# Kernel optimization log

Measured on AMD Instinct MI355X. Metric: run time of the kernel, lower is better.

Reference implementation:

```python
import jax, jax.numpy as jnp
import numpy as np
import math

B, S, H, DK, NB = 2, 128, 4, 128, 4
D = H * DK  # 512


def setup_inputs() -> dict:
    key = jax.random.key(0)
    ks = jax.random.split(key, 24)
    g = lambda i, sh, std=1.0: jax.random.normal(ks[i], sh, jnp.float32) * std
    u = lambda i, sh: jax.random.uniform(ks[i], sh, jnp.float32)
    return {
        "x_m": g(0, (B, S, D)), "x_c": g(1, (B, S, D)),
        "b_m": g(2, (B, S, D)), "b_c": g(3, (B, S, D)),
        "bb_m": g(4, (B, NB, NB, D)), "bb_c": u(5, (B, NB, NB, D)),
        "p_m": g(6, (B, S, D)), "p_c": u(7, (B, S, D)),
        "W_xm": g(8, (3, D, H, DK), 0.02), "W_xc": g(9, (3, D, H, DK), 0.02),
        "W_bm": g(10, (3, D, H, DK), 0.02), "W_bc": g(11, (3, D, H, DK), 0.02),
        "Wq1_w": g(12, (DK, DK), 0.05), "Wq1_b": g(13, (DK,), 0.02),
        "Wq2_w": g(14, (DK, DK), 0.05), "Wq2_b": g(15, (DK,), 0.02),
        "Wk1_w": g(16, (DK, DK), 0.05), "Wk1_b": g(17, (DK,), 0.02),
        "Wk2_w": g(18, (DK, DK), 0.05), "Wk2_b": g(19, (DK,), 0.02),
        "mean_w": g(20, (D, D), 0.02), "mean_b": jnp.zeros((D,), jnp.float32),
        "cov_w": g(21, (D, D), 0.02), "cov_b": jnp.zeros((D,), jnp.float32),
        "ln_w": jnp.ones((D,), jnp.float32), "ln_b": jnp.zeros((D,), jnp.float32),
        "b_seq": jax.random.randint(ks[22], (B, S), 0, NB),
    }


def _elu1(x):
    return jax.nn.elu(x) + 1.0


def _tri_sagp(m1, m2, m3, c1, c2, c3):
    # fuse three diagonal Gaussians by product-of-Gaussians (precision-weighted)
    eps = 1e-24
    p1 = 1.0 / jnp.clip(c1, eps)
    p2 = 1.0 / jnp.clip(c2, eps)
    p3 = 1.0 / jnp.clip(c3, eps)
    c = 1.0 / (p1 + p2 + p3)
    return c * (m1 * p1 + m2 * p2 + m3 * p3), c


def _ln(x, w, b):
    m = jnp.mean(x, -1, keepdims=True)
    v = jnp.mean((x - m) ** 2, -1, keepdims=True)
    return (x - m) / jnp.sqrt(v + 1e-12) * w + b


def _forward(x_m, x_c, b_m, b_c, bb_m, bb_c, p_m, p_c,
             W_xm, W_xc, W_bm, W_bc,
             Wq1_w, Wq1_b, Wq2_w, Wq2_b, Wk1_w, Wk1_b, Wk2_w, Wk2_b,
             mean_w, mean_b, cov_w, cov_b, ln_w, ln_b, b_seq):
    Bb, Ss, Dd = x_m.shape
    Hh, Dk = W_xm.shape[2], W_xm.shape[3]
    proj = lambda x, w: jnp.einsum('bnd,dhk->bhnk', x, w)
    q1 = proj(x_m, W_xm[0]) + proj(b_m, W_bm[0])
    k1 = proj(x_m, W_xm[1]) + proj(b_m, W_bm[1])
    v1 = proj(x_m, W_xm[2]) + proj(b_m, W_bm[2])
    q2 = _elu1(proj(x_c, W_xc[0]) + proj(b_c, W_bc[0]))
    k2 = _elu1(proj(x_c, W_xc[1]) + proj(b_c, W_bc[1]))
    v2 = _elu1(proj(x_c, W_xc[2]) + proj(b_c, W_bc[2]))
    nb = bb_m.shape[1]
    # [B,NB,NB,D] -> [B,H,NB,NB,DK]
    bbm = bb_m.reshape(Bb, nb, nb, Hh, Dk).transpose(0, 3, 1, 2, 4)
    bbc = bb_c.reshape(Bb, nb, nb, Hh, Dk).transpose(0, 3, 1, 2, 4)
    # out[b,h,i,j,:] = bbm[b,h,b_seq[b,j],b_seq[b,i],:]  (matches torch advanced indexing + permute)
    gather = jax.vmap(lambda bb, seq: bb[:, seq[None, :], seq[:, None], :])
    bbm_b = gather(bbm, b_seq)  # [B,H,S,S,DK]
    bbc_b = gather(bbc, b_seq)
    pm = p_m.reshape(Bb, Ss, Hh, Dk).transpose(0, 2, 1, 3)  # [B,H,S,DK]
    pc = p_c.reshape(Bb, Ss, Hh, Dk).transpose(0, 2, 1, 3)
    lin = lambda x, w, b: x @ w.T + b
    fQm, fQc = _tri_sagp(q1[:, :, :, None, :], lin(bbm_b, Wq1_w, Wq1_b),
                         lin(pm, Wq2_w, Wq2_b)[:, :, :, None, :],
                         q2[:, :, :, None, :], bbc_b, pc[:, :, :, None, :])
    fKm, fKc = _tri_sagp(k1[:, :, None, :, :], lin(bbm_b, Wk1_w, Wk1_b),
                         lin(pm, Wk2_w, Wk2_b)[:, :, None, :, :],
                         k2[:, :, None, :, :], bbc_b, pc[:, :, None, :, :])
    eps = 1e-24
    # 2-Wasserstein^2 between diagonal Gaussians (the 1x1 matmul form reduces to this)
    w2 = jnp.sum((fQm - fKm) ** 2, -1) + jnp.sum(
        (jnp.sqrt(jnp.clip(fQc, eps)) - jnp.sqrt(jnp.clip(fKc, eps))) ** 2, -1)
    scores = -w2 / math.sqrt(Dk)  # [B,H,S,S]
    probs = jax.nn.softmax(scores, axis=-1)
    mean_ctx = jnp.einsum('bhij,bhjk->bhik', probs, v1)
    cov_ctx = jnp.einsum('bhij,bhjk->bhik', probs ** 2, v2)
    mean_ctx = mean_ctx.transpose(0, 2, 1, 3).reshape(Bb, Ss, Dd)
    cov_ctx = cov_ctx.transpose(0, 2, 1, 3).reshape(Bb, Ss, Dd)
    mean_h = _ln(mean_ctx @ mean_w.T + mean_b + x_m, ln_w, ln_b)
    cov_h = _ln(cov_ctx @ cov_w.T + cov_b + x_c, ln_w, ln_b)
    return mean_h, cov_h, probs


def reference(x_m, x_c, b_m, b_c, bb_m, bb_c, p_m, p_c,
              W_xm, W_xc, W_bm, W_bc,
              Wq1_w, Wq1_b, Wq2_w, Wq2_b, Wk1_w, Wk1_b, Wk2_w, Wk2_b,
              mean_w, mean_b, cov_w, cov_b, ln_w, ln_b, b_seq):
    return _forward(x_m, x_c, b_m, b_c, bb_m, bb_c, p_m, p_c,
                    W_xm, W_xc, W_bm, W_bc,
                    Wq1_w, Wq1_b, Wq2_w, Wq2_b, Wk1_w, Wk1_b, Wk2_w, Wk2_b,
                    mean_w, mean_b, cov_w, cov_b, ln_w, ln_b, b_seq)
```

## Files before the change

kernel.cpp:

```cpp
#include <hip/hip_runtime.h>
#include <math.h>

#define B_ 2
#define S_ 128
#define H_ 4
#define DK_ 128
#define NB_ 4
#define D_ 512
#define M_ 256

typedef __attribute__((ext_vector_type(8))) short short8;
typedef __attribute__((ext_vector_type(4))) float float4v;

__device__ __forceinline__ float elu1(float x) {
    return (x > 0.f) ? (x + 1.f) : __expf(x);
}

__device__ __forceinline__ unsigned short f2bf(float f) {
    unsigned u = __float_as_uint(f);
    unsigned r = (u + 0x7FFFu + ((u >> 16) & 1u)) >> 16;
    return (unsigned short)r;
}


__global__ __launch_bounds__(256) void k_cvt_copy(
    const float* __restrict__ x_m, const float* __restrict__ b_m,
    const float* __restrict__ x_c, const float* __restrict__ b_c,
    const float* __restrict__ mean_w, const float* __restrict__ cov_w,
    unsigned short* __restrict__ A_m, unsigned short* __restrict__ A_c,
    unsigned short* __restrict__ wm_bf, unsigned short* __restrict__ wc_bf)
{
    const int t = threadIdx.x, job = blockIdx.y;
#pragma unroll
    for (int u = 0; u < 4; ++u) {
        int e = blockIdx.x * 1024 + u * 256 + t;
        float v;
        unsigned short* dst;
        if (job == 0) {
            int m = e >> 10, k = e & 1023;
            v = (k < 512) ? x_m[m * 512 + k] : b_m[m * 512 + k - 512];
            dst = A_m;
        } else if (job == 1) {
            int m = e >> 10, k = e & 1023;
            v = (k < 512) ? x_c[m * 512 + k] : b_c[m * 512 + k - 512];
            dst = A_c;
        } else if (job == 2) { v = mean_w[e]; dst = wm_bf; }
        else                 { v = cov_w[e];  dst = wc_bf; }
        dst[e] = f2bf(v);
    }
}

__global__ __launch_bounds__(256) void k_cvt_wt(
    const float* __restrict__ W_xm, const float* __restrict__ W_xc,
    const float* __restrict__ W_bm, const float* __restrict__ W_bc,
    unsigned short* __restrict__ Wt)
{
    const int o = blockIdx.z >> 1, part = blockIdx.z & 1;
    const float* src;
    if (part == 0) src = (o < 3) ? (W_xm + o * 262144) : (W_xc + (o - 3) * 262144);
    else           src = (o < 3) ? (W_bm + o * 262144) : (W_bc + (o - 3) * 262144);

    __shared__ unsigned short tile[32][33];
    const int tx = threadIdx.x & 31, ty = threadIdx.x >> 5;
    const int nt = blockIdx.x, kt = blockIdx.y;
#pragma unroll
    for (int u = 0; u < 4; ++u)
        tile[ty + u * 8][tx] = f2bf(src[(kt * 32 + ty + u * 8) * 512 + nt * 32 + tx]);
    __syncthreads();
    unsigned short* dst = Wt + o * 524288 + part * 512;
#pragma unroll
    for (int u = 0; u < 4; ++u)
        dst[(nt * 32 + ty + u * 8) * 1024 + kt * 32 + tx] = tile[tx][ty + u * 8];
}

__global__ __launch_bounds__(256) void k_mm(
    const unsigned short* __restrict__ A_m, const unsigned short* __restrict__ A_c,
    const unsigned short* __restrict__ Wt, float* __restrict__ qkv)
{
    const int t = threadIdx.x;
    const int wid = blockIdx.x * 4 + (t >> 6);
    const int lane = t & 63;
    const int o = wid >> 9;
    const int rem = wid & 511;
    const int nt = rem & 31, mt = rem >> 5;
    const int m0 = mt * 16, n0 = nt * 16;
    const int l15 = lane & 15, quad = lane >> 4;

    const unsigned short* A = (o < 3) ? A_m : A_c;
    const unsigned short* ap = A + (m0 + l15) * 1024 + quad * 8;
    const unsigned short* bp = Wt + o * 524288 + (n0 + l15) * 1024 + quad * 8;

    float4v acc0 = {0.f, 0.f, 0.f, 0.f};
    float4v acc1 = {0.f, 0.f, 0.f, 0.f};
#pragma unroll
    for (int k0 = 0; k0 < 1024; k0 += 64) {
        short8 a0 = *(const short8*)(ap + k0);
        short8 b0 = *(const short8*)(bp + k0);
        short8 a1 = *(const short8*)(ap + k0 + 32);
        short8 b1 = *(const short8*)(bp + k0 + 32);
        acc0 = __builtin_amdgcn_mfma_f32_16x16x32_bf16(a0, b0, acc0, 0, 0, 0);
        acc1 = __builtin_amdgcn_mfma_f32_16x16x32_bf16(a1, b1, acc1, 0, 0, 0);
    }

    float* dst = qkv + o * 131072;
#pragma unroll
    for (int r = 0; r < 4; ++r) {
        float v = acc0[r] + acc1[r];
        if (o >= 3) v = elu1(v);
        dst[(m0 + quad * 4 + r) * 512 + n0 + l15] = v;
    }
}

__global__ __launch_bounds__(128) void k_lin(
    const float* __restrict__ p_m, const float* __restrict__ bb_m,
    const float* __restrict__ Wq2, const float* __restrict__ bq2,
    const float* __restrict__ Wk2, const float* __restrict__ bk2,
    const float* __restrict__ Wq1, const float* __restrict__ bq1,
    const float* __restrict__ Wk1, const float* __restrict__ bk1,
    float* __restrict__ pq, float* __restrict__ pk,
    float* __restrict__ bbq, float* __restrict__ bbk)
{
    const int bx = blockIdx.x, t = threadIdx.x;
    const float *src, *Wm, *bias;
    float* dst;
    int row0;
    if (bx < 128)      { src = p_m;  Wm = Wq2; bias = bq2; dst = pq;  row0 = bx * 8; }
    else if (bx < 256) { src = p_m;  Wm = Wk2; bias = bk2; dst = pk;  row0 = (bx - 128) * 8; }
    else if (bx < 272) { src = bb_m; Wm = Wq1; bias = bq1; dst = bbq; row0 = (bx - 256) * 8; }
    else               { src = bb_m; Wm = Wk1; bias = bk1; dst = bbk; row0 = (bx - 272) * 8; }

    __shared__ float ps[8][128];
    __shared__ float wsh[128][33];

#pragma unroll
    for (int r = 0; r < 8; ++r) ps[r][t] = src[(row0 + r) * 128 + t];

    float acc[8];
#pragma unroll
    for (int r = 0; r < 8; ++r) acc[r] = 0.f;

    const int kc = t & 31, kr0 = t >> 5;
    for (int c0 = 0; c0 < 128; c0 += 32) {
        __syncthreads();
#pragma unroll 8
        for (int u = 0; u < 32; ++u)
            wsh[kr0 + u * 4][kc] = Wm[(kr0 + u * 4) * 128 + c0 + kc];
        __syncthreads();
#pragma unroll 8
        for (int k2 = 0; k2 < 32; ++k2) {
            float wv = wsh[t][k2];
#pragma unroll
            for (int r = 0; r < 8; ++r)
                acc[r] = fmaf(ps[r][c0 + k2], wv, acc[r]);
        }
    }

    float bv = bias[t];
#pragma unroll
    for (int r = 0; r < 8; ++r) dst[(row0 + r) * 128 + t] = acc[r] + bv;
}

__global__ __launch_bounds__(128) void k_fuse(
    const float* __restrict__ qkv, const float* __restrict__ pq,
    const float* __restrict__ pk, const float* __restrict__ bbq,
    const float* __restrict__ bbk, const float* __restrict__ bb_c,
    const float* __restrict__ p_c, const int* __restrict__ b_seq,
    float* __restrict__ fQm, float* __restrict__ fQs,
    float* __restrict__ fKm, float* __restrict__ fKs)
{
    const int t = threadIdx.x;
    const int ij = blockIdx.x;
    const int h = blockIdx.y;
    const int b = blockIdx.z >> 1;
    const int side = blockIdx.z & 1;
    const int d = h * 128 + t;
    const float eps = 1e-24f;
    const int base = (b * S_ + ij) * D_ + d;
    const int s_self = b_seq[b * S_ + ij];

    float m1, c1, m3;
    if (side == 0) { m1 = qkv[base];           c1 = qkv[3 * M_ * D_ + base]; m3 = pq[base]; }
    else           { m1 = qkv[M_ * D_ + base]; c1 = qkv[4 * M_ * D_ + base]; m3 = pk[base]; }
    float c3 = p_c[base];

    float p1 = 1.f / fmaxf(c1, eps);
    float p3 = 1.f / fmaxf(c3, eps);
    float mp13 = m1 * p1 + m3 * p3;
    const float* bbM = side ? bbk : bbq;

#pragma unroll
    for (int sv = 0; sv < 4; ++sv) {
        int n1 = side ? s_self : sv;
        int n2 = side ? sv : s_self;
        int idx = (b * 16 + n1 * 4 + n2) * 512 + d;
        float m2 = bbM[idx];
        float c2 = bb_c[idx];
        float p2 = 1.f / fmaxf(c2, eps);
        float cc = 1.f / (p1 + p2 + p3);
        float fm = cc * (mp13 + m2 * p2);
        float fs = sqrtf(fmaxf(cc, eps));
        if (side == 0) {
            int o = ((b * H_ + h) * S_ + ij) * 512 + sv * 128 + t;
            fQm[o] = fm; fQs[o] = fs;
        } else {
            int o = (((b * H_ + h) * 4 + sv) * S_ + ij) * 128 + t;
            fKm[o] = fm; fKs[o] = fs;
        }
    }
}

__global__ __launch_bounds__(128) void k_attn(
    const float* __restrict__ fQm, const float* __restrict__ fQs,
    const float* __restrict__ fKm, const float* __restrict__ fKs,
    const float* __restrict__ qkv, const int* __restrict__ b_seq,
    float* __restrict__ probs_out, unsigned short* __restrict__ mctxb,
    unsigned short* __restrict__ cctxb)
{
    const int t = threadIdx.x;
    const int i = blockIdx.x, h = blockIdx.y, b = blockIdx.z;

    __shared__ __attribute__((aligned(16))) float qm[4 * 132];
    __shared__ __attribute__((aligned(16))) float qs[4 * 132];
    __shared__ float red[4];
    __shared__ float pr[128], pr2[128];

    const int si = b_seq[b * S_ + i];
    const int sj = b_seq[b * S_ + t];
    const int qbase = ((b * H_ + h) * S_ + i) * 512;
#pragma unroll
    for (int u = 0; u < 4; ++u) {
        qm[u * 132 + t] = fQm[qbase + u * 128 + t];
        qs[u * 132 + t] = fQs[qbase + u * 128 + t];
    }
    __syncthreads();

    const int krow = (((b * H_ + h) * 4 + si) * S_ + t) * 128;
    const float4* kmp = (const float4*)(fKm + krow);
    const float4* ksp = (const float4*)(fKs + krow);

    float w2 = 0.f;
#pragma unroll 4
    for (int k4 = 0; k4 < 32; ++k4) {
        float4 km = kmp[k4];
        float4 ks = ksp[k4];
        float4 m = *(const float4*)&qm[sj * 132 + k4 * 4];
        float4 s = *(const float4*)&qs[sj * 132 + k4 * 4];
        float d0 = m.x - km.x, d1 = m.y - km.y, d2 = m.z - km.z, d3 = m.w - km.w;
        float e0 = s.x - ks.x, e1 = s.y - ks.y, e2 = s.z - ks.z, e3 = s.w - ks.w;
        w2 += d0 * d0 + d1 * d1 + d2 * d2 + d3 * d3
            + e0 * e0 + e1 * e1 + e2 * e2 + e3 * e3;
    }
    float score = -w2 * 0.08838834764831845f;

    float mx = score;
#pragma unroll
    for (int off = 32; off >= 1; off >>= 1) mx = fmaxf(mx, __shfl_xor(mx, off));
    if ((t & 63) == 0) red[t >> 6] = mx;
    __syncthreads();
    mx = fmaxf(red[0], red[1]);
    float e = __expf(score - mx);
    float sm = e;
#pragma unroll
    for (int off = 32; off >= 1; off >>= 1) sm += __shfl_xor(sm, off);
    if ((t & 63) == 0) red[2 + (t >> 6)] = sm;
    __syncthreads();
    float p = e / (red[2] + red[3]);

    probs_out[((b * H_ + h) * S_ + i) * S_ + t] = p;
    pr[t] = p;
    pr2[t] = p * p;
    __syncthreads();

    const float* v1 = qkv + 2 * M_ * D_ + (b * S_) * D_ + h * 128 + t;
    const float* v2 = qkv + 5 * M_ * D_ + (b * S_) * D_ + h * 128 + t;
    float am = 0.f, ac = 0.f;
#pragma unroll 8
    for (int j = 0; j < 128; ++j) {
        am = fmaf(pr[j], v1[j * D_], am);
        ac = fmaf(pr2[j], v2[j * D_], ac);
    }
    mctxb[(b * S_ + i) * D_ + h * 128 + t] = f2bf(am);
    cctxb[(b * S_ + i) * D_ + h * 128 + t] = f2bf(ac);
}

__global__ __launch_bounds__(256) void k_fin_mm(
    const unsigned short* __restrict__ mctxb, const unsigned short* __restrict__ cctxb,
    const unsigned short* __restrict__ wm_bf, const unsigned short* __restrict__ wc_bf,
    float* __restrict__ y_m, float* __restrict__ y_c)
{
    const int t = threadIdx.x;
    const int wid = blockIdx.x * 4 + (t >> 6);
    const int lane = t & 63;
    const int mat = wid >> 10;
    const int rem = wid & 1023;
    const int ks = rem >> 9;
    const int r2 = rem & 511;
    const int nt = r2 & 31, mt = r2 >> 5;
    const int m0 = mt * 16, n0 = nt * 16, kbase = ks * 256;
    const int l15 = lane & 15, quad = lane >> 4;

    const unsigned short* A = mat ? cctxb : mctxb;
    const unsigned short* Bw = mat ? wc_bf : wm_bf;
    float* y = mat ? y_c : y_m;

    const unsigned short* ap = A + (m0 + l15) * 512 + kbase + quad * 8;
    const unsigned short* bp = Bw + (n0 + l15) * 512 + kbase + quad * 8;

    float4v acc0 = {0.f, 0.f, 0.f, 0.f};
    float4v acc1 = {0.f, 0.f, 0.f, 0.f};
#pragma unroll
    for (int k0 = 0; k0 < 256; k0 += 64) {
        short8 a0 = *(const short8*)(ap + k0);
        short8 b0 = *(const short8*)(bp + k0);
        short8 a1 = *(const short8*)(ap + k0 + 32);
        short8 b1 = *(const short8*)(bp + k0 + 32);
        acc0 = __builtin_amdgcn_mfma_f32_16x16x32_bf16(a0, b0, acc0, 0, 0, 0);
        acc1 = __builtin_amdgcn_mfma_f32_16x16x32_bf16(a1, b1, acc1, 0, 0, 0);
    }
#pragma unroll
    for (int r = 0; r < 4; ++r)
        atomicAdd(&y[(m0 + quad * 4 + r) * 512 + n0 + l15], acc0[r] + acc1[r]);
}

__global__ __launch_bounds__(256) void k_ln(
    const float* __restrict__ y_m, const float* __restrict__ y_c,
    const float* __restrict__ mean_b, const float* __restrict__ cov_b,
    const float* __restrict__ x_m, const float* __restrict__ x_c,
    const float* __restrict__ ln_w, const float* __restrict__ ln_b,
    float* __restrict__ out)
{
    const int t = threadIdx.x;
    const int id = blockIdx.x;
    const int mat = id >> 8, row = id & 255;
    const float* yg = mat ? y_c : y_m;
    const float* bias = mat ? cov_b : mean_b;
    const float* res = mat ? x_c : x_m;
    const int base = row * 512;

    __shared__ float red[8];

    float y0 = yg[base + t] + bias[t] + res[base + t];
    float y1 = yg[base + 256 + t] + bias[256 + t] + res[base + 256 + t];
    float s = y0 + y1, ss = y0 * y0 + y1 * y1;
#pragma unroll
    for (int off = 32; off >= 1; off >>= 1) { s += __shfl_xor(s, off); ss += __shfl_xor(ss, off); }
    if ((t & 63) == 0) { red[t >> 6] = s; red[4 + (t >> 6)] = ss; }
    __syncthreads();
    float mu = (red[0] + red[1] + red[2] + red[3]) * (1.f / 512.f);
    float var = (red[4] + red[5] + red[6] + red[7]) * (1.f / 512.f) - mu * mu;
    float rstd = 1.f / sqrtf(var + 1e-12f);
    out[mat * 131072 + base + t] = (y0 - mu) * rstd * ln_w[t] + ln_b[t];
    out[mat * 131072 + base + 256 + t] = (y1 - mu) * rstd * ln_w[256 + t] + ln_b[256 + t];
}

extern "C" void kernel_launch(void* const* d_in, const int* in_sizes, int n_in,
                              void* d_out, int out_size, void* d_ws, size_t ws_size,
                              hipStream_t stream) {
    (void)in_sizes; (void)n_in; (void)out_size; (void)ws_size;
    const float* x_m   = (const float*)d_in[0];
    const float* x_c   = (const float*)d_in[1];
    const float* b_m   = (const float*)d_in[2];
    const float* b_c   = (const float*)d_in[3];
    const float* bb_m  = (const float*)d_in[4];
    const float* bb_c  = (const float*)d_in[5];
    const float* p_m   = (const float*)d_in[6];
    const float* p_c   = (const float*)d_in[7];
    const float* W_xm  = (const float*)d_in[8];
    const float* W_xc  = (const float*)d_in[9];
    const float* W_bm  = (const float*)d_in[10];
    const float* W_bc  = (const float*)d_in[11];
    const float* Wq1_w = (const float*)d_in[12];
    const float* Wq1_b = (const float*)d_in[13];
    const float* Wq2_w = (const float*)d_in[14];
    const float* Wq2_b = (const float*)d_in[15];
    const float* Wk1_w = (const float*)d_in[16];
    const float* Wk1_b = (const float*)d_in[17];
    const float* Wk2_w = (const float*)d_in[18];
    const float* Wk2_b = (const float*)d_in[19];
    const float* mean_w = (const float*)d_in[20];
    const float* mean_b = (const float*)d_in[21];
    const float* cov_w  = (const float*)d_in[22];
    const float* cov_b  = (const float*)d_in[23];
    const float* ln_w   = (const float*)d_in[24];
    const float* ln_b   = (const float*)d_in[25];
    const int*   b_seq  = (const int*)d_in[26];

    float* ws   = (float*)d_ws;
    float* qkv  = ws;
    float* pq   = ws + 786432;
    float* pk   = ws + 917504;
    float* bbq  = ws + 1048576;
    float* bbk  = ws + 1064960;
    float* fQm  = ws + 1081344;
    float* fQs  = ws + 1605632;
    float* fKm  = ws + 2129920;
    float* fKs  = ws + 2654208;
    float* y_m  = ws + 3178496;
    float* y_c  = ws + 3309568;
    unsigned short* A_m   = (unsigned short*)(ws + 3440640);
    unsigned short* A_c   = (unsigned short*)(ws + 3571712);
    unsigned short* Wt    = (unsigned short*)(ws + 3702784);
    unsigned short* wm_bf = (unsigned short*)(ws + 5275648);
    unsigned short* wc_bf = (unsigned short*)(ws + 5406720);
    unsigned short* mctxb = (unsigned short*)(ws + 5537792);
    unsigned short* cctxb = (unsigned short*)(ws + 5603328);
    float* out  = (float*)d_out;

    hipMemsetAsync(y_m, 0, 262144 * sizeof(float), stream);
    k_cvt_copy<<<dim3(256, 4), 256, 0, stream>>>(x_m, b_m, x_c, b_c, mean_w, cov_w,
                                                 A_m, A_c, wm_bf, wc_bf);
    k_cvt_wt<<<dim3(16, 16, 12), 256, 0, stream>>>(W_xm, W_xc, W_bm, W_bc, Wt);
    k_mm<<<dim3(768), 256, 0, stream>>>(A_m, A_c, Wt, qkv);
    k_lin<<<dim3(288), 128, 0, stream>>>(p_m, bb_m, Wq2_w, Wq2_b, Wk2_w, Wk2_b,
                                         Wq1_w, Wq1_b, Wk1_w, Wk1_b, pq, pk, bbq, bbk);
    k_fuse<<<dim3(128, 4, 4), 128, 0, stream>>>(qkv, pq, pk, bbq, bbk, bb_c, p_c, b_seq,
                                                fQm, fQs, fKm, fKs);
    k_attn<<<dim3(128, 4, 2), 128, 0, stream>>>(fQm, fQs, fKm, fKs, qkv, b_seq,
                                                out + 262144, mctxb, cctxb);
    k_fin_mm<<<dim3(512), 256, 0, stream>>>(mctxb, cctxb, wm_bf, wc_bf, y_m, y_c);
    k_ln<<<dim3(512), 256, 0, stream>>>(y_m, y_c, mean_b, cov_b, x_m, x_c,
                                        ln_w, ln_b, out);
}
```

Measured before the change: 193.7 us.

## Merge prep kernels, fold Gaussian fusion into attention, fuse output GEMM with LayerNorm

Three conversion and projection kernels become a single prep kernel. The fused Q/K Gaussian computation now runs inside the attention kernel instead of going through fQm/fQs/fKm/fKs buffers in global memory. The split-K atomic output GEMM, the memset and the LayerNorm kernel are replaced by one kernel that computes whole rows in shared memory and normalises them. This cuts launch count and global round-trips. In exchange, K-side fusion is recomputed per query (128x more reciprocal/sqrt work), and the final GEMM now runs on only 32 blocks.

```diff
diff --git a/kernel.cpp b/kernel.cpp
--- a/kernel.cpp
+++ b/kernel.cpp
@@ -23,54 +23,110 @@
 }
 
 
-__global__ __launch_bounds__(256) void k_cvt_copy(
+union __attribute__((aligned(16))) PrepSMem {
+    unsigned short tile[32][33];
+    struct { float ps[2][8][128]; float wsh[2][128][33]; } c;
+};
+
+__global__ __launch_bounds__(256) void k_prep(
     const float* __restrict__ x_m, const float* __restrict__ b_m,
     const float* __restrict__ x_c, const float* __restrict__ b_c,
     const float* __restrict__ mean_w, const float* __restrict__ cov_w,
-    unsigned short* __restrict__ A_m, unsigned short* __restrict__ A_c,
-    unsigned short* __restrict__ wm_bf, unsigned short* __restrict__ wc_bf)
-{
-    const int t = threadIdx.x, job = blockIdx.y;
-#pragma unroll
-    for (int u = 0; u < 4; ++u) {
-        int e = blockIdx.x * 1024 + u * 256 + t;
-        float v;
-        unsigned short* dst;
-        if (job == 0) {
-            int m = e >> 10, k = e & 1023;
-            v = (k < 512) ? x_m[m * 512 + k] : b_m[m * 512 + k - 512];
-            dst = A_m;
-        } else if (job == 1) {
-            int m = e >> 10, k = e & 1023;
-            v = (k < 512) ? x_c[m * 512 + k] : b_c[m * 512 + k - 512];
-            dst = A_c;
-        } else if (job == 2) { v = mean_w[e]; dst = wm_bf; }
-        else                 { v = cov_w[e];  dst = wc_bf; }
-        dst[e] = f2bf(v);
-    }
-}
-
-__global__ __launch_bounds__(256) void k_cvt_wt(
     const float* __restrict__ W_xm, const float* __restrict__ W_xc,
     const float* __restrict__ W_bm, const float* __restrict__ W_bc,
-    unsigned short* __restrict__ Wt)
+    const float* __restrict__ p_m, const float* __restrict__ bb_m,
+    const float* __restrict__ Wq2, const float* __restrict__ bq2,
+    const float* __restrict__ Wk2, const float* __restrict__ bk2,
+    const float* __restrict__ Wq1, const float* __restrict__ bq1,
+    const float* __restrict__ Wk1, const float* __restrict__ bk1,
+    unsigned short* __restrict__ A_m, unsigned short* __restrict__ A_c,
+    unsigned short* __restrict__ wm_bf, unsigned short* __restrict__ wc_bf,
+    unsigned short* __restrict__ Wt,
+    float* __restrict__ pq, float* __restrict__ pk,
+    float* __restrict__ bbq, float* __restrict__ bbk)
 {
-    const int o = blockIdx.z >> 1, part = blockIdx.z & 1;
-    const float* src;
-    if (part == 0) src = (o < 3) ? (W_xm + o * 262144) : (W_xc + (o - 3) * 262144);
-    else           src = (o < 3) ? (W_bm + o * 262144) : (W_bc + (o - 3) * 262144);
-
-    __shared__ unsigned short tile[32][33];
-    const int tx = threadIdx.x & 31, ty = threadIdx.x >> 5;
-    const int nt = blockIdx.x, kt = blockIdx.y;
-#pragma unroll
-    for (int u = 0; u < 4; ++u)
-        tile[ty + u * 8][tx] = f2bf(src[(kt * 32 + ty + u * 8) * 512 + nt * 32 + tx]);
-    __syncthreads();
-    unsigned short* dst = Wt + o * 524288 + part * 512;
-#pragma unroll
-    for (int u = 0; u < 4; ++u)
-        dst[(nt * 32 + ty + u * 8) * 1024 + kt * 32 + tx] = tile[tx][ty + u * 8];
+    __shared__ PrepSMem sm;
+    const int t = threadIdx.x;
+    const int blk = blockIdx.x;
+    const int u2 = t >> 7, tl = t & 127;
+
+    {
+        const int gid = blk * 256 + t;
+#pragma unroll
+        for (int u = 0; u < 16; ++u) {
+            int e = u * 65536 + gid;
+            int job = e >> 18, off = e & 262143;
+            float v; unsigned short* dst;
+            if (job == 0) {
+                int m = off >> 10, k = off & 1023;
+                v = (k < 512) ? x_m[m * 512 + k] : b_m[m * 512 + k - 512];
+                dst = A_m;
+            } else if (job == 1) {
+                int m = off >> 10, k = off & 1023;
+                v = (k < 512) ? x_c[m * 512 + k] : b_c[m * 512 + k - 512];
+                dst = A_c;
+            } else if (job == 2) { v = mean_w[off]; dst = wm_bf; }
+            else                 { v = cov_w[off];  dst = wc_bf; }
+            dst[off] = f2bf(v);
+        }
+    }
+    {
+        const int tx = t & 31, ty = t >> 5;
+        for (int it = 0; it < 12; ++it) {
+            int tid = blk * 12 + it;
+            int nt = tid & 15, kt = (tid >> 4) & 15, z = tid >> 8;
+            int o = z >> 1, part = z & 1;
+            const float* src;
+            if (part == 0) src = (o < 3) ? (W_xm + o * 262144) : (W_xc + (o - 3) * 262144);
+            else           src = (o < 3) ? (W_bm + o * 262144) : (W_bc + (o - 3) * 262144);
+            __syncthreads();
+#pragma unroll
+            for (int u = 0; u < 4; ++u)
+                sm.tile[ty + u * 8][tx] = f2bf(src[(kt * 32 + ty + u * 8) * 512 + nt * 32 + tx]);
+            __syncthreads();
+            unsigned short* dst = Wt + o * 524288 + part * 512;
+#pragma unroll
+            for (int u = 0; u < 4; ++u)
+                dst[(nt * 32 + ty + u * 8) * 1024 + kt * 32 + tx] = sm.tile[tx][ty + u * 8];
+        }
+    }
+    __syncthreads();
+    if (blk < 144) {
+        const int cunit = blk * 2 + u2;
+        const float *src, *Wm, *bias; float* dst; int row0;
+        if (cunit < 128)      { src = p_m;  Wm = Wq2; bias = bq2; dst = pq;  row0 = cunit * 8; }
+        else if (cunit < 256) { src = p_m;  Wm = Wk2; bias = bk2; dst = pk;  row0 = (cunit - 128) * 8; }
+        else if (cunit < 272) { src = bb_m; Wm = Wq1; bias = bq1; dst = bbq; row0 = (cunit - 256) * 8; }
+        else                  { src = bb_m; Wm = Wk1; bias = bk1; dst = bbk; row0 = (cunit - 272) * 8; }
+
+        float (*ps)[128] = sm.c.ps[u2];
+        float (*wsh)[33] = sm.c.wsh[u2];
+#pragma unroll
+        for (int r = 0; r < 8; ++r) ps[r][tl] = src[(row0 + r) * 128 + tl];
+
+        float acc[8];
+#pragma unroll
+        for (int r = 0; r < 8; ++r) acc[r] = 0.f;
+
+        const int kc = tl & 31, kr0 = tl >> 5;
+        for (int c0 = 0; c0 < 128; c0 += 32) {
+            __syncthreads();
+#pragma unroll 8
+            for (int u = 0; u < 32; ++u)
+                wsh[kr0 + u * 4][kc] = Wm[(kr0 + u * 4) * 128 + c0 + kc];
+            __syncthreads();
+#pragma unroll 8
+            for (int k2 = 0; k2 < 32; ++k2) {
+                float wvv = wsh[tl][k2];
+#pragma unroll
+                for (int r = 0; r < 8; ++r)
+                    acc[r] = fmaf(ps[r][c0 + k2], wvv, acc[r]);
+            }
+        }
+        float bv = bias[tl];
+#pragma unroll
+        for (int r = 0; r < 8; ++r) dst[(row0 + r) * 128 + tl] = acc[r] + bv;
+    }
 }
 
 __global__ __launch_bounds__(256) void k_mm(
@@ -111,113 +167,17 @@
     }
 }
 
-__global__ __launch_bounds__(128) void k_lin(
-    const float* __restrict__ p_m, const float* __restrict__ bb_m,
-    const float* __restrict__ Wq2, const float* __restrict__ bq2,
-    const float* __restrict__ Wk2, const float* __restrict__ bk2,
-    const float* __restrict__ Wq1, const float* __restrict__ bq1,
-    const float* __restrict__ Wk1, const float* __restrict__ bk1,
-    float* __restrict__ pq, float* __restrict__ pk,
-    float* __restrict__ bbq, float* __restrict__ bbk)
-{
-    const int bx = blockIdx.x, t = threadIdx.x;
-    const float *src, *Wm, *bias;
-    float* dst;
-    int row0;
-    if (bx < 128)      { src = p_m;  Wm = Wq2; bias = bq2; dst = pq;  row0 = bx * 8; }
-    else if (bx < 256) { src = p_m;  Wm = Wk2; bias = bk2; dst = pk;  row0 = (bx - 128) * 8; }
-    else if (bx < 272) { src = bb_m; Wm = Wq1; bias = bq1; dst = bbq; row0 = (bx - 256) * 8; }
-    else               { src = bb_m; Wm = Wk1; bias = bk1; dst = bbk; row0 = (bx - 272) * 8; }
-
-    __shared__ float ps[8][128];
-    __shared__ float wsh[128][33];
-
-#pragma unroll
-    for (int r = 0; r < 8; ++r) ps[r][t] = src[(row0 + r) * 128 + t];
-
-    float acc[8];
-#pragma unroll
-    for (int r = 0; r < 8; ++r) acc[r] = 0.f;
-
-    const int kc = t & 31, kr0 = t >> 5;
-    for (int c0 = 0; c0 < 128; c0 += 32) {
-        __syncthreads();
-#pragma unroll 8
-        for (int u = 0; u < 32; ++u)
-            wsh[kr0 + u * 4][kc] = Wm[(kr0 + u * 4) * 128 + c0 + kc];
-        __syncthreads();
-#pragma unroll 8
-        for (int k2 = 0; k2 < 32; ++k2) {
-            float wv = wsh[t][k2];
-#pragma unroll
-            for (int r = 0; r < 8; ++r)
-                acc[r] = fmaf(ps[r][c0 + k2], wv, acc[r]);
-        }
-    }
-
-    float bv = bias[t];
-#pragma unroll
-    for (int r = 0; r < 8; ++r) dst[(row0 + r) * 128 + t] = acc[r] + bv;
-}
-
-__global__ __launch_bounds__(128) void k_fuse(
+__global__ __launch_bounds__(128) void k_attn2(
     const float* __restrict__ qkv, const float* __restrict__ pq,
     const float* __restrict__ pk, const float* __restrict__ bbq,
     const float* __restrict__ bbk, const float* __restrict__ bb_c,
     const float* __restrict__ p_c, const int* __restrict__ b_seq,
-    float* __restrict__ fQm, float* __restrict__ fQs,
-    float* __restrict__ fKm, float* __restrict__ fKs)
-{
-    const int t = threadIdx.x;
-    const int ij = blockIdx.x;
-    const int h = blockIdx.y;
-    const int b = blockIdx.z >> 1;
-    const int side = blockIdx.z & 1;
-    const int d = h * 128 + t;
-    const float eps = 1e-24f;
-    const int base = (b * S_ + ij) * D_ + d;
-    const int s_self = b_seq[b * S_ + ij];
-
-    float m1, c1, m3;
-    if (side == 0) { m1 = qkv[base];           c1 = qkv[3 * M_ * D_ + base]; m3 = pq[base]; }
-    else           { m1 = qkv[M_ * D_ + base]; c1 = qkv[4 * M_ * D_ + base]; m3 = pk[base]; }
-    float c3 = p_c[base];
-
-    float p1 = 1.f / fmaxf(c1, eps);
-    float p3 = 1.f / fmaxf(c3, eps);
-    float mp13 = m1 * p1 + m3 * p3;
-    const float* bbM = side ? bbk : bbq;
-
-#pragma unroll
-    for (int sv = 0; sv < 4; ++sv) {
-        int n1 = side ? s_self : sv;
-        int n2 = side ? sv : s_self;
-        int idx = (b * 16 + n1 * 4 + n2) * 512 + d;
-        float m2 = bbM[idx];
-        float c2 = bb_c[idx];
-        float p2 = 1.f / fmaxf(c2, eps);
-        float cc = 1.f / (p1 + p2 + p3);
-        float fm = cc * (mp13 + m2 * p2);
-        float fs = sqrtf(fmaxf(cc, eps));
-        if (side == 0) {
-            int o = ((b * H_ + h) * S_ + ij) * 512 + sv * 128 + t;
-            fQm[o] = fm; fQs[o] = fs;
-        } else {
-            int o = (((b * H_ + h) * 4 + sv) * S_ + ij) * 128 + t;
-            fKm[o] = fm; fKs[o] = fs;
-        }
-    }
-}
-
-__global__ __launch_bounds__(128) void k_attn(
-    const float* __restrict__ fQm, const float* __restrict__ fQs,
-    const float* __restrict__ fKm, const float* __restrict__ fKs,
-    const float* __restrict__ qkv, const int* __restrict__ b_seq,
     float* __restrict__ probs_out, unsigned short* __restrict__ mctxb,
     unsigned short* __restrict__ cctxb)
 {
     const int t = threadIdx.x;
     const int i = blockIdx.x, h = blockIdx.y, b = blockIdx.z;
+    const float eps = 1e-24f;
 
     __shared__ __attribute__((aligned(16))) float qm[4 * 132];
     __shared__ __attribute__((aligned(16))) float qs[4 * 132];
@@ -226,29 +186,67 @@
 
     const int si = b_seq[b * S_ + i];
     const int sj = b_seq[b * S_ + t];
-    const int qbase = ((b * H_ + h) * S_ + i) * 512;
-#pragma unroll
-    for (int u = 0; u < 4; ++u) {
-        qm[u * 132 + t] = fQm[qbase + u * 128 + t];
-        qs[u * 132 + t] = fQs[qbase + u * 128 + t];
-    }
-    __syncthreads();
-
-    const int krow = (((b * H_ + h) * 4 + si) * S_ + t) * 128;
-    const float4* kmp = (const float4*)(fKm + krow);
-    const float4* ksp = (const float4*)(fKs + krow);
+
+    {
+        const int d = h * 128 + t;
+        const int base = (b * S_ + i) * D_ + d;
+        float m1 = qkv[base];
+        float c1 = qkv[3 * M_ * D_ + base];
+        float m3 = pq[base];
+        float c3 = p_c[base];
+        float p1 = 1.f / fmaxf(c1, eps);
+        float p3 = 1.f / fmaxf(c3, eps);
+        float mp13 = m1 * p1 + m3 * p3;
+#pragma unroll
+        for (int sv = 0; sv < 4; ++sv) {
+            int idx = (b * 16 + sv * 4 + si) * 512 + d;
+            float m2 = bbq[idx];
+            float c2 = bb_c[idx];
+            float p2 = 1.f / fmaxf(c2, eps);
+            float cc = 1.f / (p1 + p2 + p3);
+            qm[sv * 132 + t] = cc * (mp13 + m2 * p2);
+            qs[sv * 132 + t] = sqrtf(fmaxf(cc, eps));
+        }
+    }
+    __syncthreads();
+
+    const int jbase = (b * S_ + t) * D_ + h * 128;
+    const float4* k1p = (const float4*)(qkv + M_ * D_ + jbase);
+    const float4* k2p = (const float4*)(qkv + 4 * M_ * D_ + jbase);
+    const float4* pkp = (const float4*)(pk + jbase);
+    const float4* pcp = (const float4*)(p_c + jbase);
+    const int tb = (b * 16 + sj * 4 + si) * 512 + h * 128;
+    const float4* bkp = (const float4*)(bbk + tb);
+    const float4* bcp = (const float4*)(bb_c + tb);
 
     float w2 = 0.f;
 #pragma unroll 4
     for (int k4 = 0; k4 < 32; ++k4) {
-        float4 km = kmp[k4];
-        float4 ks = ksp[k4];
-        float4 m = *(const float4*)&qm[sj * 132 + k4 * 4];
-        float4 s = *(const float4*)&qs[sj * 132 + k4 * 4];
-        float d0 = m.x - km.x, d1 = m.y - km.y, d2 = m.z - km.z, d3 = m.w - km.w;
-        float e0 = s.x - ks.x, e1 = s.y - ks.y, e2 = s.z - ks.z, e3 = s.w - ks.w;
-        w2 += d0 * d0 + d1 * d1 + d2 * d2 + d3 * d3
-            + e0 * e0 + e1 * e1 + e2 * e2 + e3 * e3;
+        float4 m1v = k1p[k4];
+        float4 c1v = k2p[k4];
+        float4 m3v = pkp[k4];
+        float4 c3v = pcp[k4];
+        float4 m2v = bkp[k4];
+        float4 c2v = bcp[k4];
+        float4 qmv = *(const float4*)&qm[sj * 132 + k4 * 4];
+        float4 qsv = *(const float4*)&qs[sj * 132 + k4 * 4];
+        float dd[4], ee[4];
+#pragma unroll
+        for (int c = 0; c < 4; ++c) {
+            float m1 = ((const float*)&m1v)[c], c1 = ((const float*)&c1v)[c];
+            float m3 = ((const float*)&m3v)[c], c3 = ((const float*)&c3v)[c];
+            float m2 = ((const float*)&m2v)[c], c2 = ((const float*)&c2v)[c];
+            float p1 = 1.f / fmaxf(c1, eps);
+            float p2 = 1.f / fmaxf(c2, eps);
+            float p3 = 1.f / fmaxf(c3, eps);
+            float cc = 1.f / (p1 + p2 + p3);
+            float fm = cc * (m1 * p1 + m2 * p2 + m3 * p3);
+            float fs = sqrtf(fmaxf(cc, eps));
+            dd[c] = ((const float*)&qmv)[c] - fm;
+            ee[c] = ((const float*)&qsv)[c] - fs;
+        }
+        w2 += dd[0] * dd[0] + dd[1] * dd[1] + dd[2] * dd[2] + dd[3] * dd[3]
+            + ee[0] * ee[0] + ee[1] * ee[1] + ee[2] * ee[2] + ee[3] * ee[3];
     }
     float score = -w2 * 0.08838834764831845f;
 
@@ -283,74 +281,74 @@
     cctxb[(b * S_ + i) * D_ + h * 128 + t] = f2bf(ac);
 }
 
-__global__ __launch_bounds__(256) void k_fin_mm(
+__global__ __launch_bounds__(256) void k_fin(
     const unsigned short* __restrict__ mctxb, const unsigned short* __restrict__ cctxb,
     const unsigned short* __restrict__ wm_bf, const unsigned short* __restrict__ wc_bf,
-    float* __restrict__ y_m, float* __restrict__ y_c)
-{
-    const int t = threadIdx.x;
-    const int wid = blockIdx.x * 4 + (t >> 6);
-    const int lane = t & 63;
-    const int mat = wid >> 10;
-    const int rem = wid & 1023;
-    const int ks = rem >> 9;
-    const int r2 = rem & 511;
-    const int nt = r2 & 31, mt = r2 >> 5;
-    const int m0 = mt * 16, n0 = nt * 16, kbase = ks * 256;
-    const int l15 = lane & 15, quad = lane >> 4;
-
-    const unsigned short* A = mat ? cctxb : mctxb;
-    const unsigned short* Bw = mat ? wc_bf : wm_bf;
-    float* y = mat ? y_c : y_m;
-
-    const unsigned short* ap = A + (m0 + l15) * 512 + kbase + quad * 8;
-    const unsigned short* bp = Bw + (n0 + l15) * 512 + kbase + quad * 8;
-
-    float4v acc0 = {0.f, 0.f, 0.f, 0.f};
-    float4v acc1 = {0.f, 0.f, 0.f, 0.f};
-#pragma unroll
-    for (int k0 = 0; k0 < 256; k0 += 64) {
-        short8 a0 = *(const short8*)(ap + k0);
-        short8 b0 = *(const short8*)(bp + k0);
-        short8 a1 = *(const short8*)(ap + k0 + 32);
-        short8 b1 = *(const short8*)(bp + k0 + 32);
-        acc0 = __builtin_amdgcn_mfma_f32_16x16x32_bf16(a0, b0, acc0, 0, 0, 0);
-        acc1 = __builtin_amdgcn_mfma_f32_16x16x32_bf16(a1, b1, acc1, 0, 0, 0);
-    }
-#pragma unroll
-    for (int r = 0; r < 4; ++r)
-        atomicAdd(&y[(m0 + quad * 4 + r) * 512 + n0 + l15], acc0[r] + acc1[r]);
-}
-
-__global__ __launch_bounds__(256) void k_ln(
-    const float* __restrict__ y_m, const float* __restrict__ y_c,
     const float* __restrict__ mean_b, const float* __restrict__ cov_b,
     const float* __restrict__ x_m, const float* __restrict__ x_c,
     const float* __restrict__ ln_w, const float* __restrict__ ln_b,
     float* __restrict__ out)
 {
+    const int mat = blockIdx.x >> 4, mt = blockIdx.x & 15;
+    const int m0 = mt * 16;
+    const unsigned short* A = mat ? cctxb : mctxb;
+    const unsigned short* Bw = mat ? wc_bf : wm_bf;
+
+    __shared__ float y[16][516];
+
     const int t = threadIdx.x;
-    const int id = blockIdx.x;
-    const int mat = id >> 8, row = id & 255;
-    const float* yg = mat ? y_c : y_m;
+    const int wv = t >> 6, lane = t & 63;
+    const int l15 = lane & 15, quad = lane >> 4;
+
+    const unsigned short* ap = A + (m0 + l15) * 512 + quad * 8;
+#pragma unroll
+    for (int u = 0; u < 8; ++u) {
+        int n0 = (wv * 8 + u) * 16;
+        const unsigned short* bp = Bw + (n0 + l15) * 512 + quad * 8;
+        float4v acc0 = {0.f, 0.f, 0.f, 0.f};
+        float4v acc1 = {0.f, 0.f, 0.f, 0.f};
+#pragma unroll
+        for (int k0 = 0; k0 < 512; k0 += 64) {
+            short8 a0 = *(const short8*)(ap + k0);
+            short8 b0 = *(const short8*)(bp + k0);
+            short8 a1 = *(const short8*)(ap + k0 + 32);
+            short8 b1 = *(const short8*)(bp + k0 + 32);
+            acc0 = __builtin_amdgcn_mfma_f32_16x16x32_bf16(a0, b0, acc0, 0, 0, 0);
+            acc1 = __builtin_amdgcn_mfma_f32_16x16x32_bf16(a1, b1, acc1, 0, 0, 0);
+        }
+#pragma unroll
+        for (int r = 0; r < 4; ++r)
+            y[quad * 4 + r][n0 + l15] = acc0[r] + acc1[r];
+    }
+    __syncthreads();
+
+    const int r = t >> 4, c = t & 15;
+    const int row = m0 + r;
     const float* bias = mat ? cov_b : mean_b;
     const float* res = mat ? x_c : x_m;
-    const int base = row * 512;
-
-    __shared__ float red[8];
-
-    float y0 = yg[base + t] + bias[t] + res[base + t];
-    float y1 = yg[base + 256 + t] + bias[256 + t] + res[base + 256 + t];
-    float s = y0 + y1, ss = y0 * y0 + y1 * y1;
-#pragma unroll
-    for (int off = 32; off >= 1; off >>= 1) { s += __shfl_xor(s, off); ss += __shfl_xor(ss, off); }
-    if ((t & 63) == 0) { red[t >> 6] = s; red[4 + (t >> 6)] = ss; }
-    __syncthreads();
-    float mu = (red[0] + red[1] + red[2] + red[3]) * (1.f / 512.f);
-    float var = (red[4] + red[5] + red[6] + red[7]) * (1.f / 512.f) - mu * mu;
+
+    float vals[32];
+    float s = 0.f, ss = 0.f;
+#pragma unroll
+    for (int u = 0; u < 32; ++u) {
+        int col = c + 16 * u;
+        float v = y[r][col] + bias[col] + res[row * 512 + col];
+        vals[u] = v;
+        s += v; ss += v * v;
+    }
+#pragma unroll
+    for (int off = 8; off >= 1; off >>= 1) {
+        s += __shfl_xor(s, off);
+        ss += __shfl_xor(ss, off);
+    }
+    float mu = s * (1.f / 512.f);
+    float var = ss * (1.f / 512.f) - mu * mu;
     float rstd = 1.f / sqrtf(var + 1e-12f);
-    out[mat * 131072 + base + t] = (y0 - mu) * rstd * ln_w[t] + ln_b[t];
-    out[mat * 131072 + base + 256 + t] = (y1 - mu) * rstd * ln_w[256 + t] + ln_b[256 + t];
+#pragma unroll
+    for (int u = 0; u < 32; ++u) {
+        int col = c + 16 * u;
+        out[mat * 131072 + row * 512 + col] = (vals[u] - mu) * rstd * ln_w[col] + ln_b[col];
+    }
 }
 
 extern "C" void kernel_launch(void* const* d_in, const int* in_sizes, int n_in,
@@ -385,39 +383,28 @@
     const float* ln_b   = (const float*)d_in[25];
     const int*   b_seq  = (const int*)d_in[26];
 
-    float* ws   = (float*)d_ws;
-    float* qkv  = ws;
-    float* pq   = ws + 786432;
-    float* pk   = ws + 917504;
-    float* bbq  = ws + 1048576;
-    float* bbk  = ws + 1064960;
-    float* fQm  = ws + 1081344;
-    float* fQs  = ws + 1605632;
-    float* fKm  = ws + 2129920;
-    float* fKs  = ws + 2654208;
-    float* y_m  = ws + 3178496;
-    float* y_c  = ws + 3309568;
-    unsigned short* A_m   = (unsigned short*)(ws + 3440640);
-    unsigned short* A_c   = (unsigned short*)(ws + 3571712);
-    unsigned short* Wt    = (unsigned short*)(ws + 3702784);
-    unsigned short* wm_bf = (unsigned short*)(ws + 5275648);
-    unsigned short* wc_bf = (unsigned short*)(ws + 5406720);
-    unsigned short* mctxb = (unsigned short*)(ws + 5537792);
-    unsigned short* cctxb = (unsigned short*)(ws + 5603328);
-    float* out  = (float*)d_out;
-
-    hipMemsetAsync(y_m, 0, 262144 * sizeof(float), stream);
-    k_cvt_copy<<<dim3(256, 4), 256, 0, stream>>>(x_m, b_m, x_c, b_c, mean_w, cov_w,
-                                                 A_m, A_c, wm_bf, wc_bf);
-    k_cvt_wt<<<dim3(16, 16, 12), 256, 0, stream>>>(W_xm, W_xc, W_bm, W_bc, Wt);
+    float* ws = (float*)d_ws;
+    float* qkv = ws;
+    float* pq  = ws + 786432;
+    float* pk  = ws + 917504;
+    float* bbq = ws + 1048576;
+    float* bbk = ws + 1064960;
+    unsigned short* A_m   = (unsigned short*)(ws + 1081344);
+    unsigned short* A_c   = (unsigned short*)(ws + 1212416);
+    unsigned short* Wt    = (unsigned short*)(ws + 1343488);
+    unsigned short* wm_bf = (unsigned short*)(ws + 2916352);
+    unsigned short* wc_bf = (unsigned short*)(ws + 3047424);
+    unsigned short* mctxb = (unsigned short*)(ws + 3178496);
+    unsigned short* cctxb = (unsigned short*)(ws + 3244032);
+    float* out = (float*)d_out;
+
+    k_prep<<<dim3(256), 256, 0, stream>>>(
+        x_m, b_m, x_c, b_c, mean_w, cov_w, W_xm, W_xc, W_bm, W_bc,
+        p_m, bb_m, Wq2_w, Wq2_b, Wk2_w, Wk2_b, Wq1_w, Wq1_b, Wk1_w, Wk1_b,
+        A_m, A_c, wm_bf, wc_bf, Wt, pq, pk, bbq, bbk);
     k_mm<<<dim3(768), 256, 0, stream>>>(A_m, A_c, Wt, qkv);
-    k_lin<<<dim3(288), 128, 0, stream>>>(p_m, bb_m, Wq2_w, Wq2_b, Wk2_w, Wk2_b,
-                                         Wq1_w, Wq1_b, Wk1_w, Wk1_b, pq, pk, bbq, bbk);
-    k_fuse<<<dim3(128, 4, 4), 128, 0, stream>>>(qkv, pq, pk, bbq, bbk, bb_c, p_c, b_seq,
-                                                fQm, fQs, fKm, fKs);
-    k_attn<<<dim3(128, 4, 2), 128, 0, stream>>>(fQm, fQs, fKm, fKs, qkv, b_seq,
-                                                out + 262144, mctxb, cctxb);
-    k_fin_mm<<<dim3(512), 256, 0, stream>>>(mctxb, cctxb, wm_bf, wc_bf, y_m, y_c);
-    k_ln<<<dim3(512), 256, 0, stream>>>(y_m, y_c, mean_b, cov_b, x_m, x_c,
-                                        ln_w, ln_b, out);
-}
+    k_attn2<<<dim3(128, 4, 2), 128, 0, stream>>>(
+        qkv, pq, pk, bbq, bbk, bb_c, p_c, b_seq, out + 262144, mctxb, cctxb);
+    k_fin<<<dim3(32), 256, 0, stream>>>(
+        mctxb, cctxb, wm_bf, wc_bf, mean_b, cov_b, x_m, x_c, ln_w, ln_b, out);
+}
```

Result: slower. 257.5 us (+32.9%).
